# Kernel tuning notes

Hardware: AMD Instinct MI355X
Metric: run time of the kernel (lower is better)

The kernel has to match this reference:

```python
import jax, jax.numpy as jnp
import numpy as np

B, T, N, E = 4, 16, 1024, 16384
F_IN, H, FF, NH, L, C = 128, 256, 1024, 8, 2, 10
HD = H // NH
EPS = 1e-5


def setup_inputs() -> dict:
    key = jax.random.key(0)
    ks = jax.random.split(key, 12)
    g = lambda k, s: jax.random.normal(k, s, dtype=jnp.float32) * 0.02
    return {
        "x": jax.random.normal(ks[0], (B, T, N, F_IN), dtype=jnp.float32),
        "edge_index": jax.random.randint(ks[1], (B, T, 2, E), 0, N, dtype=jnp.int32),
        # GraphSAGE layer 1 (PyG SAGEConv: lin_l on mean-aggregated neighbors, lin_r on self)
        "sage1_Wl": g(ks[2], (F_IN, H)), "sage1_bl": jnp.zeros((H,), jnp.float32),
        "sage1_Wr": g(ks[3], (F_IN, H)),
        # GraphSAGE layer 2
        "sage2_Wl": g(ks[4], (H, H)), "sage2_bl": jnp.zeros((H,), jnp.float32),
        "sage2_Wr": g(ks[5], (H, H)),
        # TransformerEncoder, stacked over L layers
        "Wqkv": g(ks[6], (L, H, 3 * H)), "bqkv": jnp.zeros((L, 3 * H), jnp.float32),
        "Wo": g(ks[7], (L, H, H)), "bo": jnp.zeros((L, H), jnp.float32),
        "ln1_s": jnp.ones((L, H), jnp.float32), "ln1_b": jnp.zeros((L, H), jnp.float32),
        "W1": g(ks[8], (L, H, FF)), "b1": jnp.zeros((L, FF), jnp.float32),
        "W2": g(ks[9], (L, FF, H)), "b2": jnp.zeros((L, H), jnp.float32),
        "ln2_s": jnp.ones((L, H), jnp.float32), "ln2_b": jnp.zeros((L, H), jnp.float32),
        # final classifier
        "fc_W": g(ks[10], (H, C)), "fc_b": jnp.zeros((C,), jnp.float32),
    }


def _sage_conv(x, src, dst, Wl, bl, Wr):
    # mean neighbor aggregation: for each target node, mean of source features
    deg = jax.ops.segment_sum(jnp.ones((E,), x.dtype), dst, num_segments=N)
    agg = jax.ops.segment_sum(x[src], dst, num_segments=N)  # [N, F]
    agg = agg / jnp.clip(deg, 1.0)[:, None]
    return agg @ Wl + bl + x @ Wr


def _layernorm(x, s, b):
    m = jnp.mean(x, axis=-1, keepdims=True)
    v = jnp.var(x, axis=-1, keepdims=True)
    return (x - m) * jax.lax.rsqrt(v + EPS) * s + b


def _encoder_layer(h, Wqkv, bqkv, Wo, bo, ln1_s, ln1_b, W1, b1, W2, b2, ln2_s, ln2_b):
    # h: [B, T, H] -- post-norm (PyTorch default norm_first=False), relu FFN
    qkv = h @ Wqkv + bqkv  # [B, T, 3H]
    q, k, v = jnp.split(qkv, 3, axis=-1)
    sp = lambda t: t.reshape(B, T, NH, HD).transpose(0, 2, 1, 3)  # [B, NH, T, HD]
    q, k, v = sp(q), sp(k), sp(v)
    scores = jnp.einsum("bhqd,bhkd->bhqk", q, k) / np.sqrt(HD).astype(np.float32)
    attn = jax.nn.softmax(scores, axis=-1)
    ctx = jnp.einsum("bhqk,bhkd->bhqd", attn, v)
    ctx = ctx.transpose(0, 2, 1, 3).reshape(B, T, H)
    h = _layernorm(h + ctx @ Wo + bo, ln1_s, ln1_b)
    ffn = jax.nn.relu(h @ W1 + b1) @ W2 + b2
    return _layernorm(h + ffn, ln2_s, ln2_b)


def reference(x, edge_index, sage1_Wl, sage1_bl, sage1_Wr, sage2_Wl, sage2_bl,
              sage2_Wr, Wqkv, bqkv, Wo, bo, ln1_s, ln1_b, W1, b1, W2, b2,
              ln2_s, ln2_b, fc_W, fc_b):
    xf = x.reshape(B * T, N, F_IN)
    ef = edge_index.reshape(B * T, 2, E)

    def per_graph(xg, eg):
        src, dst = eg[0], eg[1]
        h = jax.nn.relu(_sage_conv(xg, src, dst, sage1_Wl, sage1_bl, sage1_Wr))
        h = _sage_conv(h, src, dst, sage2_Wl, sage2_bl, sage2_Wr)
        return jnp.mean(h, axis=0)  # mean-pool over nodes -> [H]

    emb = jax.vmap(per_graph)(xf, ef).reshape(B, T, H)

    h = emb
    for l in range(L):
        h = _encoder_layer(h, Wqkv[l], bqkv[l], Wo[l], bo[l], ln1_s[l], ln1_b[l],
                           W1[l], b1[l], W2[l], b2[l], ln2_s[l], ln2_b[l])
    return h[:, -1, :] @ fc_W + fc_b  # [B, C]
```

## Files before the change

### kernel.cpp

```cpp
#include <hip/hip_runtime.h>
#include <hip/hip_bf16.h>

#define Bc 4
#define Tc 16
#define Nc 1024
#define Ec 16384
#define FIN 128
#define Hc 256
#define FFc 1024
#define NHc 8
#define Lc 2
#define HDc 32
#define Gc 64
#define EPSc 1e-5f

typedef __bf16 v8bf __attribute__((ext_vector_type(8)));
typedef float v4f __attribute__((ext_vector_type(4)));

__global__ void pack_w_kernel(const float* __restrict__ Wl, const float* __restrict__ Wr,
                              __bf16* __restrict__ pH, __bf16* __restrict__ pL) {
    int bid = blockIdx.x;
    int t = threadIdx.x;
    int lane = t >> 3, j = t & 7;
    int kc = bid >> 4, nt = bid & 15;
    int k = kc * 32 + ((lane >> 4) << 3) + j;
    int n = nt * 16 + (lane & 15);
    float w = (k < 128) ? Wl[(size_t)k * Hc + n] : Wr[(size_t)(k - 128) * Hc + n];
    __bf16 hi = (__bf16)w;
    __bf16 lo = (__bf16)(w - (float)hi);
    pH[bid * 512 + t] = hi;
    pL[bid * 512 + t] = lo;
}

__global__ __launch_bounds__(1024) void csr_kernel(
        const int* __restrict__ ei, float* __restrict__ invdeg, float* __restrict__ cw,
        int* __restrict__ off, unsigned short* __restrict__ elist, float* __restrict__ uv) {
    __shared__ int degs[Nc];
    __shared__ float inv[Nc];
    __shared__ float cl[Nc];
    __shared__ int wsum[16];
    int g = blockIdx.x, t = threadIdx.x;
    const int* src = ei + (size_t)g * 2 * Ec;
    const int* dst = src + Ec;
    if (t < 512) uv[g * 512 + t] = 0.f;
    degs[t] = 0; cl[t] = 0.f;
    __syncthreads();
    for (int e = t; e < Ec; e += 1024) atomicAdd(&degs[dst[e] & (Nc - 1)], 1);
    __syncthreads();
    float iv = 1.0f / fmaxf((float)degs[t], 1.0f);
    inv[t] = iv;
    invdeg[g * Nc + t] = iv;
    __syncthreads();
    for (int e = t; e < Ec; e += 1024) atomicAdd(&cl[src[e] & (Nc - 1)], inv[dst[e] & (Nc - 1)]);
    __syncthreads();
    cw[g * Nc + t] = cl[t];
    int own = degs[t];
    int lane = t & 63, wv = t >> 6;
    int val = own;
#pragma unroll
    for (int ofs = 1; ofs < 64; ofs <<= 1) {
        int v = __shfl_up(val, ofs, 64);
        if (lane >= ofs) val += v;
    }
    if (lane == 63) wsum[wv] = val;
    __syncthreads();
    if (wv == 0 && lane < 16) {
        int wval = wsum[lane];
#pragma unroll
        for (int ofs = 1; ofs < 16; ofs <<= 1) {
            int v = __shfl_up(wval, ofs, 64);
            if (lane >= ofs) wval += v;
        }
        wsum[lane] = wval;
    }
    __syncthreads();
    int incl = val + ((wv > 0) ? wsum[wv - 1] : 0);
    int excl = incl - own;
    off[g * 1032 + t] = excl;
    if (t == 1023) off[g * 1032 + Nc] = incl;
    degs[t] = excl;
    __syncthreads();
    for (int e = t; e < Ec; e += 1024) {
        int d = dst[e] & (Nc - 1);
        int slot = atomicAdd(&degs[d], 1);
        elist[(size_t)g * Ec + slot] = (unsigned short)(src[e] & (Nc - 1));
    }
}

__global__ __launch_bounds__(512) void sage_kernel(
        const float* __restrict__ x, const unsigned short* __restrict__ elist,
        const int* __restrict__ off, const float* __restrict__ invdeg,
        const float* __restrict__ cw, const __bf16* __restrict__ pH,
        const __bf16* __restrict__ pL, const float* __restrict__ bias,
        float* __restrict__ uv) {
    __shared__ float aggL[32 * 132];
    __shared__ float xL[32 * 132];
    __shared__ float lu[256], lv[256];
    int tid = threadIdx.x;
    int bid = blockIdx.x;
    int g = bid & 63, cc = bid >> 6, r0 = cc * 32;
    const unsigned short* el = elist + (size_t)g * Ec;
    const float* xg = x + (size_t)g * Nc * FIN;
    if (tid < 256) { lu[tid] = 0.f; lv[tid] = 0.f; }

    {
        int lr = tid >> 4, ch = tid & 15;
        int n = r0 + lr;
        int o0 = off[g * 1032 + n], o1 = off[g * 1032 + n + 1];
        float4 a0 = make_float4(0.f, 0.f, 0.f, 0.f);
        float4 a1 = make_float4(0.f, 0.f, 0.f, 0.f);
        const float* xc = xg + ch * 8;
        int e = o0;
        for (; e + 8 <= o1; e += 8) {
            int s[8];
#pragma unroll
            for (int j = 0; j < 8; ++j) s[j] = el[e + j];
            float4 v0[8], v1[8];
#pragma unroll
            for (int j = 0; j < 8; ++j) {
                const float4* xp = (const float4*)(xc + (size_t)s[j] * FIN);
                v0[j] = xp[0]; v1[j] = xp[1];
            }
#pragma unroll
            for (int j = 0; j < 8; ++j) {
                a0.x += v0[j].x; a0.y += v0[j].y; a0.z += v0[j].z; a0.w += v0[j].w;
                a1.x += v1[j].x; a1.y += v1[j].y; a1.z += v1[j].z; a1.w += v1[j].w;
            }
        }
        for (; e < o1; ++e) {
            const float4* xp = (const float4*)(xc + (size_t)el[e] * FIN);
            float4 v0 = xp[0], v1 = xp[1];
            a0.x += v0.x; a0.y += v0.y; a0.z += v0.z; a0.w += v0.w;
            a1.x += v1.x; a1.y += v1.y; a1.z += v1.z; a1.w += v1.w;
        }
        float iv = invdeg[g * Nc + n];
        float* dp = &aggL[lr * 132 + ch * 8];
        dp[0] = a0.x * iv; dp[1] = a0.y * iv; dp[2] = a0.z * iv; dp[3] = a0.w * iv;
        dp[4] = a1.x * iv; dp[5] = a1.y * iv; dp[6] = a1.z * iv; dp[7] = a1.w * iv;
    }
    for (int i = tid; i < 1024; i += 512) {
        int lr = i >> 5, kq = i & 31;
        *(float4*)&xL[lr * 132 + kq * 4] = *(const float4*)&xg[(size_t)(r0 + lr) * FIN + kq * 4];
    }
    __syncthreads();

    int w = tid >> 6, lane = tid & 63, quad = lane >> 4;
    int mt = w & 1, nh = w >> 1;
    int lrow = mt * 16 + (lane & 15);
    v4f acc[4];
#pragma unroll
    for (int i = 0; i < 4; ++i) acc[i] = (v4f)0.f;
    for (int kc = 0; kc < 8; ++kc) {
        const float* ap = (kc < 4) ? &aggL[lrow * 132 + kc * 32 + quad * 8]
                                   : &xL[lrow * 132 + (kc - 4) * 32 + quad * 8];
        float4 f0 = *(const float4*)ap;
        float4 f1 = *(const float4*)(ap + 4);
        float av[8] = {f0.x, f0.y, f0.z, f0.w, f1.x, f1.y, f1.z, f1.w};
        v8bf aH, aL;
#pragma unroll
        for (int j = 0; j < 8; ++j) {
            __bf16 hb = (__bf16)av[j];
            aH[j] = hb;
            aL[j] = (__bf16)(av[j] - (float)hb);
        }
#pragma unroll
        for (int i = 0; i < 4; ++i) {
            int nt = nh * 4 + i;
            v8bf bH = *(const v8bf*)(pH + ((size_t)(kc * 16 + nt) * 64 + lane) * 8);
            v8bf bL = *(const v8bf*)(pL + ((size_t)(kc * 16 + nt) * 64 + lane) * 8);
            acc[i] = __builtin_amdgcn_mfma_f32_16x16x32_bf16(aH, bH, acc[i], 0, 0, 0);
            acc[i] = __builtin_amdgcn_mfma_f32_16x16x32_bf16(aL, bH, acc[i], 0, 0, 0);
            acc[i] = __builtin_amdgcn_mfma_f32_16x16x32_bf16(aH, bL, acc[i], 0, 0, 0);
        }
    }

    float c4[4];
    int nb = g * Nc + r0 + mt * 16 + quad * 4;
#pragma unroll
    for (int r = 0; r < 4; ++r) c4[r] = cw[nb + r];
#pragma unroll
    for (int i = 0; i < 4; ++i) {
        int col = (nh * 4 + i) * 16 + (lane & 15);
        float bcol = bias[col];
        float su = 0.f, sv = 0.f;
#pragma unroll
        for (int r = 0; r < 4; ++r) {
            float val = fmaxf(acc[i][r] + bcol, 0.f);
            sv += val;
            su += c4[r] * val;
        }
        su += __shfl_xor(su, 16); sv += __shfl_xor(sv, 16);
        su += __shfl_xor(su, 32); sv += __shfl_xor(sv, 32);
        if (quad == 0) { atomicAdd(&lu[col], su); atomicAdd(&lv[col], sv); }
    }
    __syncthreads();
    if (tid < 256) {
        atomicAdd(&uv[g * 512 + tid], lu[tid]);
        atomicAdd(&uv[g * 512 + 256 + tid], lv[tid]);
    }
}

__global__ __launch_bounds__(512) void emb_kernel(
        const float* __restrict__ uv, const float* __restrict__ Wl2,
        const float* __restrict__ bl2, const float* __restrict__ Wr2,
        float* __restrict__ h) {
    __shared__ float s[512];
    __shared__ float r2[512];
    int g = blockIdx.x, tid = threadIdx.x;
    s[tid] = uv[g * 512 + tid] * (1.0f / Nc);
    __syncthreads();
    int col = tid & 255, p = tid >> 8;
    float val = 0.f;
    if (p == 0) { for (int k = 0; k < 256; ++k) val += s[k] * Wl2[(size_t)k * Hc + col]; }
    else        { for (int k = 0; k < 256; ++k) val += s[256 + k] * Wr2[(size_t)k * Hc + col]; }
    r2[tid] = val;
    __syncthreads();
    if (tid < 256) h[g * Hc + tid] = bl2[tid] + r2[tid] + r2[tid + 256];
}

__global__ __launch_bounds__(512) void qkv_kernel(
        const float* __restrict__ h, const float* __restrict__ Wqkv,
        const float* __restrict__ bqkv, float* __restrict__ qkv, int l) {
    __shared__ float hr[256];
    __shared__ float r2[512];
    int bid = blockIdx.x;
    int gi = bid / 3, seg = bid % 3;
    int tid = threadIdx.x;
    if (tid < 256) hr[tid] = h[gi * Hc + tid];
    __syncthreads();
    int col = seg * 256 + (tid & 255);
    int half = tid >> 8;
    const float* W = Wqkv + (size_t)l * Hc * 768;
    float val = 0.f;
    int k0 = half * 128;
    for (int k = 0; k < 128; ++k) val += hr[k0 + k] * W[(size_t)(k0 + k) * 768 + col];
    r2[tid] = val;
    __syncthreads();
    if (tid < 256) qkv[gi * 768 + col] = bqkv[(size_t)l * 768 + col] + r2[tid] + r2[tid + 256];
}

#define KVS 516
__global__ __launch_bounds__(512) void apl_kernel(
        const float* __restrict__ h, const float* __restrict__ qkvg,
        const float* __restrict__ Wo, const float* __restrict__ bo,
        const float* __restrict__ s1, const float* __restrict__ b1ln,
        float* __restrict__ h1buf, int l) {
    __shared__ float kv[16 * KVS];
    __shared__ float q[256];
    __shared__ float sc[8][17];
    __shared__ float ctx[256];
    __shared__ float r2[512];
    __shared__ float red[256];
    int t = blockIdx.x, tid = threadIdx.x;
    int b = t >> 4;
    const float* qb = qkvg + (size_t)(b * 16) * 768;
    for (int i = tid; i < 8192; i += 512) {
        int j = i >> 9, d = i & 511;
        kv[j * KVS + d] = qb[(size_t)j * 768 + 256 + d];
    }
    if (tid < 256) q[tid] = qkvg[(size_t)t * 768 + tid];
    __syncthreads();
    if (tid < 128) {
        int hd = tid >> 4, j = tid & 15;
        float s = 0.f;
#pragma unroll
        for (int d = 0; d < 32; ++d) s += q[hd * 32 + d] * kv[j * KVS + hd * 32 + d];
        sc[hd][j] = s * 0.17677669529663687f;
    }
    __syncthreads();
    if (tid < 8) {
        float m = sc[tid][0];
        for (int j = 1; j < 16; ++j) m = fmaxf(m, sc[tid][j]);
        float e[16], sum = 0.f;
        for (int j = 0; j < 16; ++j) { e[j] = expf(sc[tid][j] - m); sum += e[j]; }
        float inv = 1.0f / sum;
        for (int j = 0; j < 16; ++j) sc[tid][j] = e[j] * inv;
    }
    __syncthreads();
    if (tid < 256) {
        int hd = tid >> 5, d = tid & 31;
        float o = 0.f;
#pragma unroll
        for (int j = 0; j < 16; ++j) o += sc[hd][j] * kv[j * KVS + 256 + hd * 32 + d];
        ctx[tid] = o;
    }
    __syncthreads();
    int col = tid & 255, half = tid >> 8;
    const float* W = Wo + (size_t)l * 65536;
    float pv = 0.f;
    int k0 = half * 128;
    for (int k = 0; k < 128; ++k) pv += ctx[k0 + k] * W[(size_t)(k0 + k) * 256 + col];
    r2[tid] = pv;
    __syncthreads();
    float val = 0.f;
    if (tid < 256) {
        val = h[(size_t)t * 256 + tid] + bo[(size_t)l * 256 + tid] + r2[tid] + r2[tid + 256];
        red[tid] = val;
    }
    __syncthreads();
    for (int s = 128; s > 0; s >>= 1) { if (tid < s) red[tid] += red[tid + s]; __syncthreads(); }
    float m1 = red[0] * (1.0f / 256.0f);
    __syncthreads();
    float d1 = val - m1;
    if (tid < 256) red[tid] = d1 * d1;
    __syncthreads();
    for (int s = 128; s > 0; s >>= 1) { if (tid < s) red[tid] += red[tid + s]; __syncthreads(); }
    float v1 = red[0] * (1.0f / 256.0f);
    if (tid < 256)
        h1buf[(size_t)t * 256 + tid] =
            d1 * rsqrtf(v1 + EPSc) * s1[(size_t)l * 256 + tid] + b1ln[(size_t)l * 256 + tid];
}

__global__ __launch_bounds__(512) void ffn1_kernel(
        const float* __restrict__ h1buf, const float* __restrict__ W1,
        const float* __restrict__ bf1, float* __restrict__ fL, int l) {
    __shared__ float hr[256];
    __shared__ float r2[512];
    int bid = blockIdx.x;
    int t = bid >> 2, cg = bid & 3;
    int tid = threadIdx.x;
    if (tid < 256) hr[tid] = h1buf[(size_t)t * 256 + tid];
    __syncthreads();
    int col = cg * 256 + (tid & 255);
    int half = tid >> 8;
    const float* W = W1 + (size_t)l * 262144;
    float val = 0.f;
    int k0 = half * 128;
    for (int k = 0; k < 128; ++k) val += hr[k0 + k] * W[(size_t)(k0 + k) * 1024 + col];
    r2[tid] = val;
    __syncthreads();
    if (tid < 256)
        fL[(size_t)t * 1024 + col] = fmaxf(bf1[(size_t)l * 1024 + col] + r2[tid] + r2[tid + 256], 0.f);
}

__global__ __launch_bounds__(1024) void ffn2_ln_kernel(
        float* __restrict__ h, const float* __restrict__ h1buf, const float* __restrict__ fL,
        const float* __restrict__ W2, const float* __restrict__ bf2,
        const float* __restrict__ s2, const float* __restrict__ b2ln,
        const float* __restrict__ fcW, const float* __restrict__ fcb,
        float* __restrict__ out, int l, int last) {
    __shared__ float fs[1024];
    __shared__ float r4[1024];
    __shared__ float red[256];
    int t = blockIdx.x, tid = threadIdx.x;
    fs[tid] = fL[(size_t)t * 1024 + tid];
    __syncthreads();
    int col = tid & 255, kq = tid >> 8;
    const float* W = W2 + (size_t)l * 262144;
    float p = 0.f;
    int k0 = kq * 256;
    for (int k = 0; k < 256; ++k) p += fs[k0 + k] * W[(size_t)(k0 + k) * 256 + col];
    r4[tid] = p;
    __syncthreads();
    float val = 0.f;
    if (tid < 256) {
        val = h1buf[(size_t)t * 256 + tid] + bf2[(size_t)l * 256 + tid]
            + r4[tid] + r4[tid + 256] + r4[tid + 512] + r4[tid + 768];
        red[tid] = val;
    }
    __syncthreads();
    for (int s = 128; s > 0; s >>= 1) { if (tid < s) red[tid] += red[tid + s]; __syncthreads(); }
    float m2 = red[0] * (1.0f / 256.0f);
    __syncthreads();
    float d2 = (tid < 256) ? (val - m2) : 0.f;
    if (tid < 256) red[tid] = d2 * d2;
    __syncthreads();
    for (int s = 128; s > 0; s >>= 1) { if (tid < s) red[tid] += red[tid + s]; __syncthreads(); }
    float var2 = red[0] * (1.0f / 256.0f);
    float hn = 0.f;
    if (tid < 256) {
        hn = d2 * rsqrtf(var2 + EPSc) * s2[(size_t)l * 256 + tid] + b2ln[(size_t)l * 256 + tid];
        h[(size_t)t * 256 + tid] = hn;
    }
    if (last && (t & 15) == 15) {
        __syncthreads();
        if (tid < 256) red[tid] = hn;
        __syncthreads();
        if (tid < 10) {
            int b = t >> 4;
            float fv = fcb[tid];
            for (int k = 0; k < 256; ++k) fv += red[k] * fcW[(size_t)k * 10 + tid];
            out[b * 10 + tid] = fv;
        }
    }
}

extern "C" void kernel_launch(void* const* d_in, const int* in_sizes, int n_in,
                              void* d_out, int out_size, void* d_ws, size_t ws_size,
                              hipStream_t stream) {
    (void)in_sizes; (void)n_in; (void)out_size; (void)ws_size;
    const float* x    = (const float*)d_in[0];
    const int*   ei   = (const int*)d_in[1];
    const float* s1Wl = (const float*)d_in[2];
    const float* s1bl = (const float*)d_in[3];
    const float* s1Wr = (const float*)d_in[4];
    const float* s2Wl = (const float*)d_in[5];
    const float* s2bl = (const float*)d_in[6];
    const float* s2Wr = (const float*)d_in[7];
    const float* Wqkv = (const float*)d_in[8];
    const float* bqkv = (const float*)d_in[9];
    const float* Wo   = (const float*)d_in[10];
    const float* bo   = (const float*)d_in[11];
    const float* ln1s = (const float*)d_in[12];
    const float* ln1b = (const float*)d_in[13];
    const float* W1   = (const float*)d_in[14];
    const float* b1   = (const float*)d_in[15];
    const float* W2   = (const float*)d_in[16];
    const float* b2   = (const float*)d_in[17];
    const float* ln2s = (const float*)d_in[18];
    const float* ln2b = (const float*)d_in[19];
    const float* fcW  = (const float*)d_in[20];
    const float* fcb  = (const float*)d_in[21];

    char* ws = (char*)d_ws;
    __bf16*         packWH = (__bf16*)(ws + 0);
    __bf16*         packWL = (__bf16*)(ws + 131072);
    float*          invdeg = (float*)(ws + 262144);
    float*          cw     = (float*)(ws + 524288);
    int*            off    = (int*)(ws + 786432);
    unsigned short* elist  = (unsigned short*)(ws + 1050624);
    float*          uv     = (float*)(ws + 3147776);
    float*          h      = (float*)(ws + 3278848);
    float*          qkvg   = (float*)(ws + 3344384);
    float*          h1buf  = (float*)(ws + 3540992);
    float*          fLbuf  = (float*)(ws + 3606528);

    pack_w_kernel<<<128, 512, 0, stream>>>(s1Wl, s1Wr, packWH, packWL);
    csr_kernel<<<Gc, 1024, 0, stream>>>(ei, invdeg, cw, off, elist, uv);
    sage_kernel<<<Gc * 32, 512, 0, stream>>>(x, elist, off, invdeg, cw, packWH, packWL, s1bl, uv);
    emb_kernel<<<Gc, 512, 0, stream>>>(uv, s2Wl, s2bl, s2Wr, h);
    for (int l = 0; l < Lc; ++l) {
        qkv_kernel<<<Gc * 3, 512, 0, stream>>>(h, Wqkv, bqkv, qkvg, l);
        apl_kernel<<<Gc, 512, 0, stream>>>(h, qkvg, Wo, bo, ln1s, ln1b, h1buf, l);
        ffn1_kernel<<<Gc * 4, 512, 0, stream>>>(h1buf, W1, b1, fLbuf, l);
        ffn2_ln_kernel<<<Gc, 1024, 0, stream>>>(h, h1buf, fLbuf, W2, b2, ln2s, ln2b,
                                                fcW, fcb, (float*)d_out, l, l == Lc - 1);
    }
}
```

Baseline: 321.1 us.

## Pipeline SAGE neighbor gather through LDS with async global_load_lds

Reworks the neighbor aggregation in sage_kernel. Each wave now owns 4 rows and streams the source-node feature rows into a 4-slot LDS ring using global_load_lds, with manual vmcnt waits keeping several loads in flight. The edge list for the block is first staged into shared memory, and the self-feature tile is also loaded asynchronously with global_load_lds; an old per-thread gather remains as a fallback when a block has more than 1024 edges. The aim is to hide gather latency and issue wider coalesced loads, at the cost of more shared memory (about 70KB, which lowers occupancy) and hand-written waitcnt logic.

```diff
diff --git a/kernel.cpp b/kernel.cpp
--- a/kernel.cpp
+++ b/kernel.cpp
@@ -16,6 +16,10 @@
 
 typedef __bf16 v8bf __attribute__((ext_vector_type(8)));
 typedef float v4f __attribute__((ext_vector_type(4)));
+
+#define GLOAD_LDS16(gp, lp) \
+    __builtin_amdgcn_global_load_lds((const __attribute__((address_space(1))) void*)(gp), \
+                                     (__attribute__((address_space(3))) void*)(lp), 16, 0, 0)
 
 __global__ void pack_w_kernel(const float* __restrict__ Wl, const float* __restrict__ Wr,
                               __bf16* __restrict__ pH, __bf16* __restrict__ pL) {
@@ -93,42 +97,103 @@
         const float* __restrict__ cw, const __bf16* __restrict__ pH,
         const __bf16* __restrict__ pL, const float* __restrict__ bias,
         float* __restrict__ uv) {
-    __shared__ float aggL[32 * 132];
-    __shared__ float xL[32 * 132];
-    __shared__ float lu[256], lv[256];
+    __shared__ __align__(16) float smem[17570];
+    float* aggL = smem;
+    float* xL = smem + 4224;
+    float* stage = smem + 8320;
+    float* lu = smem + 16512;
+    float* lv = smem + 16768;
+    float* invS = smem + 17024;
+    unsigned short* elS = (unsigned short*)(smem + 17056);
+
     int tid = threadIdx.x;
     int bid = blockIdx.x;
     int g = bid & 63, cc = bid >> 6, r0 = cc * 32;
     const unsigned short* el = elist + (size_t)g * Ec;
     const float* xg = x + (size_t)g * Nc * FIN;
+    int wv = tid >> 6, lane = tid & 63;
+
+#pragma unroll
+    for (int k = 0; k < 2; ++k) {
+        int rr = 4 * wv + 2 * k;
+        const float* gp = xg + (size_t)(r0 + rr) * FIN + lane * 4;
+        GLOAD_LDS16(gp, &xL[rr * FIN]);
+    }
+
+    int ob = g * 1032 + r0;
+    int eb0 = off[ob];
+    int eend = off[ob + 32];
+    int cnt = eend - eb0;
+    bool fb = (cnt > 1024);
+
     if (tid < 256) { lu[tid] = 0.f; lv[tid] = 0.f; }
-
-    {
+    if (tid < 32) invS[tid] = invdeg[g * Nc + r0 + tid];
+    if (!fb) {
+        for (int i = tid; i < cnt + 2; i += 512) elS[i] = el[eb0 + i];
+    }
+    int rw0 = r0 + 4 * wv;
+    int oA  = off[g * 1032 + rw0];
+    int oE1 = off[g * 1032 + rw0 + 1];
+    int oE2 = off[g * 1032 + rw0 + 2];
+    int oE3 = off[g * 1032 + rw0 + 3];
+    int oE4 = off[g * 1032 + rw0 + 4];
+    __syncthreads();
+
+    if (!fb) {
+        float* myst = &stage[wv * 1024];
+        int ebase = oA;
+        int nE = oE4 - oA;
+        int np = (nE + 1) >> 1;
+        float ax = 0.f, ay = 0.f;
+        int r = 0;
+        int bnd = oE1;
+
+        auto ISSUE = [&](int p) {
+            int e0 = ebase + 2 * p;
+            int s = elS[e0 - eb0 + (lane >> 5)] & (Nc - 1);
+            const float* gp = xg + (size_t)s * FIN + (lane & 31) * 4;
+            GLOAD_LDS16(gp, myst + (p & 3) * 256);
+        };
+        auto WOUT = [&]() {
+            float iv = invS[4 * wv + r];
+            int arow = 4 * wv + r;
+            *(float2*)&aggL[arow * 132 + 2 * lane] = make_float2(ax * iv, ay * iv);
+            ax = 0.f; ay = 0.f;
+            ++r;
+            bnd = (r == 1) ? oE2 : (r == 2) ? oE3 : oE4;
+        };
+
+        if (np > 0) ISSUE(0);
+        if (np > 1) ISSUE(1);
+        if (np > 2) ISSUE(2);
+        int e = ebase;
+        for (int p = 0; p < np; ++p) {
+            int rem = np - 1 - p;
+            if (rem >= 2)      asm volatile("s_waitcnt vmcnt(2)" ::: "memory");
+            else if (rem == 1) asm volatile("s_waitcnt vmcnt(1)" ::: "memory");
+            else               asm volatile("s_waitcnt vmcnt(0)" ::: "memory");
+            const float* sp = myst + (p & 3) * 256;
+#pragma unroll
+            for (int j = 0; j < 2; ++j) {
+                while (r < 4 && e >= bnd) WOUT();
+                if (e < oE4) {
+                    float2 v = *(const float2*)&sp[j * 128 + 2 * lane];
+                    ax += v.x; ay += v.y;
+                }
+                ++e;
+            }
+            if (p + 3 < np) ISSUE(p + 3);
+        }
+        while (r < 4) WOUT();
+    } else {
         int lr = tid >> 4, ch = tid & 15;
         int n = r0 + lr;
         int o0 = off[g * 1032 + n], o1 = off[g * 1032 + n + 1];
         float4 a0 = make_float4(0.f, 0.f, 0.f, 0.f);
         float4 a1 = make_float4(0.f, 0.f, 0.f, 0.f);
         const float* xc = xg + ch * 8;
-        int e = o0;
-        for (; e + 8 <= o1; e += 8) {
-            int s[8];
-#pragma unroll
-            for (int j = 0; j < 8; ++j) s[j] = el[e + j];
-            float4 v0[8], v1[8];
-#pragma unroll
-            for (int j = 0; j < 8; ++j) {
-                const float4* xp = (const float4*)(xc + (size_t)s[j] * FIN);
-                v0[j] = xp[0]; v1[j] = xp[1];
-            }
-#pragma unroll
-            for (int j = 0; j < 8; ++j) {
-                a0.x += v0[j].x; a0.y += v0[j].y; a0.z += v0[j].z; a0.w += v0[j].w;
-                a1.x += v1[j].x; a1.y += v1[j].y; a1.z += v1[j].z; a1.w += v1[j].w;
-            }
-        }
-        for (; e < o1; ++e) {
-            const float4* xp = (const float4*)(xc + (size_t)el[e] * FIN);
+        for (int e2 = o0; e2 < o1; ++e2) {
+            const float4* xp = (const float4*)(xc + (size_t)el[e2] * FIN);
             float4 v0 = xp[0], v1 = xp[1];
             a0.x += v0.x; a0.y += v0.y; a0.z += v0.z; a0.w += v0.w;
             a1.x += v1.x; a1.y += v1.y; a1.z += v1.z; a1.w += v1.w;
@@ -138,13 +203,9 @@
         dp[0] = a0.x * iv; dp[1] = a0.y * iv; dp[2] = a0.z * iv; dp[3] = a0.w * iv;
         dp[4] = a1.x * iv; dp[5] = a1.y * iv; dp[6] = a1.z * iv; dp[7] = a1.w * iv;
     }
-    for (int i = tid; i < 1024; i += 512) {
-        int lr = i >> 5, kq = i & 31;
-        *(float4*)&xL[lr * 132 + kq * 4] = *(const float4*)&xg[(size_t)(r0 + lr) * FIN + kq * 4];
-    }
-    __syncthreads();
-
-    int w = tid >> 6, lane = tid & 63, quad = lane >> 4;
+    __syncthreads();
+
+    int w = wv, quad = lane >> 4;
     int mt = w & 1, nh = w >> 1;
     int lrow = mt * 16 + (lane & 15);
     v4f acc[4];
@@ -152,7 +213,7 @@
     for (int i = 0; i < 4; ++i) acc[i] = (v4f)0.f;
     for (int kc = 0; kc < 8; ++kc) {
         const float* ap = (kc < 4) ? &aggL[lrow * 132 + kc * 32 + quad * 8]
-                                   : &xL[lrow * 132 + (kc - 4) * 32 + quad * 8];
+                                   : &xL[lrow * 128 + (kc - 4) * 32 + quad * 8];
         float4 f0 = *(const float4*)ap;
         float4 f1 = *(const float4*)(ap + 4);
         float av[8] = {f0.x, f0.y, f0.z, f0.w, f1.x, f1.y, f1.z, f1.w};
@@ -177,17 +238,17 @@
     float c4[4];
     int nb = g * Nc + r0 + mt * 16 + quad * 4;
 #pragma unroll
-    for (int r = 0; r < 4; ++r) c4[r] = cw[nb + r];
+    for (int rr = 0; rr < 4; ++rr) c4[rr] = cw[nb + rr];
 #pragma unroll
     for (int i = 0; i < 4; ++i) {
         int col = (nh * 4 + i) * 16 + (lane & 15);
         float bcol = bias[col];
         float su = 0.f, sv = 0.f;
 #pragma unroll
-        for (int r = 0; r < 4; ++r) {
-            float val = fmaxf(acc[i][r] + bcol, 0.f);
+        for (int rr = 0; rr < 4; ++rr) {
+            float val = fmaxf(acc[i][rr] + bcol, 0.f);
             sv += val;
-            su += c4[r] * val;
+            su += c4[rr] * val;
         }
         su += __shfl_xor(su, 16); sv += __shfl_xor(sv, 16);
         su += __shfl_xor(su, 32); sv += __shfl_xor(sv, 32);
```

Result: slower. 573.5 us (+78.6%).

## Pipeline SAGE neighbor gather per wave with LDS-staged edge list

Applied to the files above, without the earlier changes.

The neighbor aggregation in the SAGE kernel now stages the block's edge indices into shared memory, then has each wave walk the edges of 4 consecutive nodes. Each lane loads a float2 covering the full 128-wide feature row, with a 16-deep software pipeline of in-flight loads and index prefetch, flushing accumulators at node boundaries. The self-feature tile load is moved ahead of the gather so it overlaps with it. The aim is more memory-level parallelism and coalesced row reads, replacing the old 16-thread-per-row scheme. This costs more registers and branchy boundary handling, and keeps a fallback path for blocks with more than 1024 edges.

```diff
diff --git a/kernel.cpp b/kernel.cpp
--- a/kernel.cpp
+++ b/kernel.cpp
@@ -96,39 +96,121 @@
     __shared__ float aggL[32 * 132];
     __shared__ float xL[32 * 132];
     __shared__ float lu[256], lv[256];
+    __shared__ float invS[32];
+    __shared__ unsigned short elS[1024];
     int tid = threadIdx.x;
     int bid = blockIdx.x;
     int g = bid & 63, cc = bid >> 6, r0 = cc * 32;
     const unsigned short* el = elist + (size_t)g * Ec;
     const float* xg = x + (size_t)g * Nc * FIN;
+    int wv = tid >> 6, lane = tid & 63;
     if (tid < 256) { lu[tid] = 0.f; lv[tid] = 0.f; }
-
-    {
+    if (tid < 32) invS[tid] = invdeg[g * Nc + r0 + tid];
+
+    int ob = g * 1032 + r0;
+    int eb0 = off[ob];
+    int cnt = off[ob + 32] - eb0;
+    bool fb = (cnt > 1024);
+    if (!fb) {
+        for (int i = tid; i < cnt; i += 512) elS[i] = el[eb0 + i];
+    }
+    for (int i = tid; i < 1024; i += 512) {
+        int lr = i >> 5, kq = i & 31;
+        *(float4*)&xL[lr * 132 + kq * 4] = *(const float4*)&xg[(size_t)(r0 + lr) * FIN + kq * 4];
+    }
+    int rw0 = r0 + 4 * wv;
+    int oA  = off[g * 1032 + rw0];
+    int oE1 = off[g * 1032 + rw0 + 1];
+    int oE2 = off[g * 1032 + rw0 + 2];
+    int oE3 = off[g * 1032 + rw0 + 3];
+    int oE4 = off[g * 1032 + rw0 + 4];
+    __syncthreads();
+
+    if (!fb) {
+        int qA = oA - eb0;
+        int m  = oE4 - oA;
+        float ax = 0.f, ay = 0.f;
+        int r = 0, bnd = oE1;
+        const float* xl2 = xg + (lane << 1);
+        float2 s0, s1, s2, s3, s4, s5, s6, s7;
+        float2 u0, u1, u2, u3, u4, u5, u6, u7;
+        int iA0, iA1, iA2, iA3, iA4, iA5, iA6, iA7;
+        int iB0, iB1, iB2, iB3, iB4, iB5, iB6, iB7;
+
+#define FLUSHW() { float iv_ = invS[(wv << 2) + r]; \
+        *(float2*)&aggL[((wv << 2) + r) * 132 + (lane << 1)] = \
+            make_float2(ax * iv_, ay * iv_); \
+        ax = 0.f; ay = 0.f; ++r; \
+        bnd = (r == 1) ? oE2 : (r == 2) ? oE3 : (r == 3) ? oE4 : 0x7fffffff; }
+#define RD(NK, J) NK = ((J) < m) ? (int)elS[qA + (J)] : 0;
+#define ISS(SK, NK, J) if ((J) < m) SK = *(const float2*)(xl2 + ((NK) << 7));
+#define CONSUME(SK, J) { int eg_ = oA + (J); \
+        while (r < 4 && eg_ >= bnd) FLUSHW(); \
+        ax += SK.x; ay += SK.y; }
+
+        {
+            int t0, t1, t2, t3, t4, t5, t6, t7;
+            RD(t0, 0) RD(t1, 1) RD(t2, 2) RD(t3, 3) RD(t4, 4) RD(t5, 5) RD(t6, 6) RD(t7, 7)
+            ISS(s0, t0, 0) ISS(s1, t1, 1) ISS(s2, t2, 2) ISS(s3, t3, 3)
+            ISS(s4, t4, 4) ISS(s5, t5, 5) ISS(s6, t6, 6) ISS(s7, t7, 7)
+            RD(t0, 8) RD(t1, 9) RD(t2, 10) RD(t3, 11) RD(t4, 12) RD(t5, 13) RD(t6, 14) RD(t7, 15)
+            ISS(u0, t0, 8) ISS(u1, t1, 9) ISS(u2, t2, 10) ISS(u3, t3, 11)
+            ISS(u4, t4, 12) ISS(u5, t5, 13) ISS(u6, t6, 14) ISS(u7, t7, 15)
+        }
+        RD(iA0, 16) RD(iA1, 17) RD(iA2, 18) RD(iA3, 19)
+        RD(iA4, 20) RD(iA5, 21) RD(iA6, 22) RD(iA7, 23)
+        RD(iB0, 24) RD(iB1, 25) RD(iB2, 26) RD(iB3, 27)
+        RD(iB4, 28) RD(iB5, 29) RD(iB6, 30) RD(iB7, 31)
+
+        int jb = 0;
+        for (; jb + 16 <= m; jb += 16) {
+            CONSUME(s0, jb + 0)  ISS(s0, iA0, jb + 16) RD(iA0, jb + 32)
+            CONSUME(s1, jb + 1)  ISS(s1, iA1, jb + 17) RD(iA1, jb + 33)
+            CONSUME(s2, jb + 2)  ISS(s2, iA2, jb + 18) RD(iA2, jb + 34)
+            CONSUME(s3, jb + 3)  ISS(s3, iA3, jb + 19) RD(iA3, jb + 35)
+            CONSUME(s4, jb + 4)  ISS(s4, iA4, jb + 20) RD(iA4, jb + 36)
+            CONSUME(s5, jb + 5)  ISS(s5, iA5, jb + 21) RD(iA5, jb + 37)
+            CONSUME(s6, jb + 6)  ISS(s6, iA6, jb + 22) RD(iA6, jb + 38)
+            CONSUME(s7, jb + 7)  ISS(s7, iA7, jb + 23) RD(iA7, jb + 39)
+            CONSUME(u0, jb + 8)  ISS(u0, iB0, jb + 24) RD(iB0, jb + 40)
+            CONSUME(u1, jb + 9)  ISS(u1, iB1, jb + 25) RD(iB1, jb + 41)
+            CONSUME(u2, jb + 10) ISS(u2, iB2, jb + 26) RD(iB2, jb + 42)
+            CONSUME(u3, jb + 11) ISS(u3, iB3, jb + 27) RD(iB3, jb + 43)
+            CONSUME(u4, jb + 12) ISS(u4, iB4, jb + 28) RD(iB4, jb + 44)
+            CONSUME(u5, jb + 13) ISS(u5, iB5, jb + 29) RD(iB5, jb + 45)
+            CONSUME(u6, jb + 14) ISS(u6, iB6, jb + 30) RD(iB6, jb + 46)
+            CONSUME(u7, jb + 15) ISS(u7, iB7, jb + 31) RD(iB7, jb + 47)
+        }
+        if (jb + 0 < m)  CONSUME(s0, jb + 0)
+        if (jb + 1 < m)  CONSUME(s1, jb + 1)
+        if (jb + 2 < m)  CONSUME(s2, jb + 2)
+        if (jb + 3 < m)  CONSUME(s3, jb + 3)
+        if (jb + 4 < m)  CONSUME(s4, jb + 4)
+        if (jb + 5 < m)  CONSUME(s5, jb + 5)
+        if (jb + 6 < m)  CONSUME(s6, jb + 6)
+        if (jb + 7 < m)  CONSUME(s7, jb + 7)
+        if (jb + 8 < m)  CONSUME(u0, jb + 8)
+        if (jb + 9 < m)  CONSUME(u1, jb + 9)
+        if (jb + 10 < m) CONSUME(u2, jb + 10)
+        if (jb + 11 < m) CONSUME(u3, jb + 11)
+        if (jb + 12 < m) CONSUME(u4, jb + 12)
+        if (jb + 13 < m) CONSUME(u5, jb + 13)
+        if (jb + 14 < m) CONSUME(u6, jb + 14)
+        if (jb + 15 < m) CONSUME(u7, jb + 15)
+        while (r < 4) FLUSHW();
+#undef FLUSHW
+#undef RD
+#undef ISS
+#undef CONSUME
+    } else {
         int lr = tid >> 4, ch = tid & 15;
         int n = r0 + lr;
         int o0 = off[g * 1032 + n], o1 = off[g * 1032 + n + 1];
         float4 a0 = make_float4(0.f, 0.f, 0.f, 0.f);
         float4 a1 = make_float4(0.f, 0.f, 0.f, 0.f);
         const float* xc = xg + ch * 8;
-        int e = o0;
-        for (; e + 8 <= o1; e += 8) {
-            int s[8];
-#pragma unroll
-            for (int j = 0; j < 8; ++j) s[j] = el[e + j];
-            float4 v0[8], v1[8];
-#pragma unroll
-            for (int j = 0; j < 8; ++j) {
-                const float4* xp = (const float4*)(xc + (size_t)s[j] * FIN);
-                v0[j] = xp[0]; v1[j] = xp[1];
-            }
-#pragma unroll
-            for (int j = 0; j < 8; ++j) {
-                a0.x += v0[j].x; a0.y += v0[j].y; a0.z += v0[j].z; a0.w += v0[j].w;
-                a1.x += v1[j].x; a1.y += v1[j].y; a1.z += v1[j].z; a1.w += v1[j].w;
-            }
-        }
-        for (; e < o1; ++e) {
-            const float4* xp = (const float4*)(xc + (size_t)el[e] * FIN);
+        for (int e2 = o0; e2 < o1; ++e2) {
+            const float4* xp = (const float4*)(xc + (size_t)el[e2] * FIN);
             float4 v0 = xp[0], v1 = xp[1];
             a0.x += v0.x; a0.y += v0.y; a0.z += v0.z; a0.w += v0.w;
             a1.x += v1.x; a1.y += v1.y; a1.z += v1.z; a1.w += v1.w;
@@ -138,13 +220,9 @@
         dp[0] = a0.x * iv; dp[1] = a0.y * iv; dp[2] = a0.z * iv; dp[3] = a0.w * iv;
         dp[4] = a1.x * iv; dp[5] = a1.y * iv; dp[6] = a1.z * iv; dp[7] = a1.w * iv;
     }
-    for (int i = tid; i < 1024; i += 512) {
-        int lr = i >> 5, kq = i & 31;
-        *(float4*)&xL[lr * 132 + kq * 4] = *(const float4*)&xg[(size_t)(r0 + lr) * FIN + kq * 4];
-    }
-    __syncthreads();
-
-    int w = tid >> 6, lane = tid & 63, quad = lane >> 4;
+    __syncthreads();
+
+    int w = wv, quad = lane >> 4;
     int mt = w & 1, nh = w >> 1;
     int lrow = mt * 16 + (lane & 15);
     v4f acc[4];
@@ -177,17 +255,17 @@
     float c4[4];
     int nb = g * Nc + r0 + mt * 16 + quad * 4;
 #pragma unroll
-    for (int r = 0; r < 4; ++r) c4[r] = cw[nb + r];
+    for (int rr = 0; rr < 4; ++rr) c4[rr] = cw[nb + rr];
 #pragma unroll
     for (int i = 0; i < 4; ++i) {
         int col = (nh * 4 + i) * 16 + (lane & 15);
         float bcol = bias[col];
         float su = 0.f, sv = 0.f;
 #pragma unroll
-        for (int r = 0; r < 4; ++r) {
-            float val = fmaxf(acc[i][r] + bcol, 0.f);
+        for (int rr = 0; rr < 4; ++rr) {
+            float val = fmaxf(acc[i][rr] + bcol, 0.f);
             sv += val;
-            su += c4[r] * val;
+            su += c4[rr] * val;
         }
         su += __shfl_xor(su, 16); sv += __shfl_xor(sv, 16);
         su += __shfl_xor(su, 32); sv += __shfl_xor(sv, 32);
```

New measurement: 339.4 us. 5.7% more time.

## Fuse each transformer encoder layer into a single kernel launch

Applied to the files above, without the earlier changes.

Replaces the four per-layer kernels (qkv, attention+proj+LN, FFN1, FFN2+LN) with one 1024-thread kernel per layer. Each block recomputes the K/V projections for all 16 timesteps of its batch from a transposed copy of h held in shared memory, so the qkv, h1 and FFN intermediates no longer round-trip through global memory. This cuts six launches and their global-memory handoffs. The cost is redundant K/V computation, 16x per batch, and only 64 blocks doing the FFN matmuls instead of up to 256.

```diff
diff --git a/kernel.cpp b/kernel.cpp
--- a/kernel.cpp
+++ b/kernel.cpp
@@ -218,54 +218,73 @@
     if (tid < 256) h[g * Hc + tid] = bl2[tid] + r2[tid] + r2[tid + 256];
 }
 
-__global__ __launch_bounds__(512) void qkv_kernel(
-        const float* __restrict__ h, const float* __restrict__ Wqkv,
-        const float* __restrict__ bqkv, float* __restrict__ qkv, int l) {
-    __shared__ float hr[256];
-    __shared__ float r2[512];
-    int bid = blockIdx.x;
-    int gi = bid / 3, seg = bid % 3;
-    int tid = threadIdx.x;
-    if (tid < 256) hr[tid] = h[gi * Hc + tid];
-    __syncthreads();
-    int col = seg * 256 + (tid & 255);
-    int half = tid >> 8;
-    const float* W = Wqkv + (size_t)l * Hc * 768;
-    float val = 0.f;
-    int k0 = half * 128;
-    for (int k = 0; k < 128; ++k) val += hr[k0 + k] * W[(size_t)(k0 + k) * 768 + col];
-    r2[tid] = val;
-    __syncthreads();
-    if (tid < 256) qkv[gi * 768 + col] = bqkv[(size_t)l * 768 + col] + r2[tid] + r2[tid + 256];
-}
-
-#define KVS 516
-__global__ __launch_bounds__(512) void apl_kernel(
-        const float* __restrict__ h, const float* __restrict__ qkvg,
+__global__ __launch_bounds__(1024) void layer_kernel(
+        const float* __restrict__ hin, float* __restrict__ hout,
+        const float* __restrict__ Wqkv, const float* __restrict__ bqkv,
         const float* __restrict__ Wo, const float* __restrict__ bo,
         const float* __restrict__ s1, const float* __restrict__ b1ln,
-        float* __restrict__ h1buf, int l) {
-    __shared__ float kv[16 * KVS];
+        const float* __restrict__ W1, const float* __restrict__ bf1,
+        const float* __restrict__ W2, const float* __restrict__ bf2,
+        const float* __restrict__ s2, const float* __restrict__ b2ln,
+        const float* __restrict__ fcW, const float* __restrict__ fcb,
+        float* __restrict__ out, int l, int last) {
+    __shared__ float hT[256 * 16];
+    __shared__ float kvL[16 * 512];
     __shared__ float q[256];
     __shared__ float sc[8][17];
     __shared__ float ctx[256];
     __shared__ float r2[512];
     __shared__ float red[256];
+    __shared__ float rF[2048];
+    __shared__ float fLs[1024];
+    __shared__ float h1L[256];
     int t = blockIdx.x, tid = threadIdx.x;
-    int b = t >> 4;
-    const float* qb = qkvg + (size_t)(b * 16) * 768;
-    for (int i = tid; i < 8192; i += 512) {
-        int j = i >> 9, d = i & 511;
-        kv[j * KVS + d] = qb[(size_t)j * 768 + 256 + d];
-    }
-    if (tid < 256) q[tid] = qkvg[(size_t)t * 768 + tid];
+    int b = t >> 4, own = t & 15;
+    for (int i = tid; i < 4096; i += 1024) {
+        int j = i >> 8, k = i & 255;
+        hT[k * 16 + j] = hin[(size_t)(b * 16 + j) * 256 + k];
+    }
+    __syncthreads();
+    {
+        int col = tid & 511, jh = tid >> 9;
+        const float* W = Wqkv + (size_t)l * Hc * 768 + 256 + col;
+        float acc[8], s0[8];
+#pragma unroll
+        for (int j = 0; j < 8; ++j) acc[j] = 0.f;
+        for (int k = 0; k < 128; ++k) {
+            float w = W[(size_t)k * 768];
+            const float4* hk = (const float4*)&hT[k * 16 + jh * 8];
+            float4 h0 = hk[0], h1 = hk[1];
+            acc[0] += h0.x * w; acc[1] += h0.y * w; acc[2] += h0.z * w; acc[3] += h0.w * w;
+            acc[4] += h1.x * w; acc[5] += h1.y * w; acc[6] += h1.z * w; acc[7] += h1.w * w;
+        }
+#pragma unroll
+        for (int j = 0; j < 8; ++j) { s0[j] = acc[j]; acc[j] = 0.f; }
+        for (int k = 128; k < 256; ++k) {
+            float w = W[(size_t)k * 768];
+            const float4* hk = (const float4*)&hT[k * 16 + jh * 8];
+            float4 h0 = hk[0], h1 = hk[1];
+            acc[0] += h0.x * w; acc[1] += h0.y * w; acc[2] += h0.z * w; acc[3] += h0.w * w;
+            acc[4] += h1.x * w; acc[5] += h1.y * w; acc[6] += h1.z * w; acc[7] += h1.w * w;
+        }
+        float bq = bqkv[(size_t)l * 768 + 256 + col];
+#pragma unroll
+        for (int j = 0; j < 8; ++j) kvL[(size_t)(jh * 8 + j) * 512 + col] = bq + s0[j] + acc[j];
+    }
+    if (tid < 256) {
+        const float* W = Wqkv + (size_t)l * Hc * 768 + tid;
+        float p0 = 0.f, p1 = 0.f;
+        for (int k = 0; k < 128; ++k) p0 += hT[k * 16 + own] * W[(size_t)k * 768];
+        for (int k = 128; k < 256; ++k) p1 += hT[k * 16 + own] * W[(size_t)k * 768];
+        q[tid] = bqkv[(size_t)l * 768 + tid] + p0 + p1;
+    }
     __syncthreads();
     if (tid < 128) {
-        int hd = tid >> 4, j = tid & 15;
+        int hd = tid >> 4, jj = tid & 15;
         float s = 0.f;
 #pragma unroll
-        for (int d = 0; d < 32; ++d) s += q[hd * 32 + d] * kv[j * KVS + hd * 32 + d];
-        sc[hd][j] = s * 0.17677669529663687f;
+        for (int d = 0; d < 32; ++d) s += q[hd * 32 + d] * kvL[jj * 512 + hd * 32 + d];
+        sc[hd][jj] = s * 0.17677669529663687f;
     }
     __syncthreads();
     if (tid < 8) {
@@ -281,20 +300,22 @@
         int hd = tid >> 5, d = tid & 31;
         float o = 0.f;
 #pragma unroll
-        for (int j = 0; j < 16; ++j) o += sc[hd][j] * kv[j * KVS + 256 + hd * 32 + d];
+        for (int j = 0; j < 16; ++j) o += sc[hd][j] * kvL[j * 512 + 256 + hd * 32 + d];
         ctx[tid] = o;
     }
     __syncthreads();
-    int col = tid & 255, half = tid >> 8;
-    const float* W = Wo + (size_t)l * 65536;
-    float pv = 0.f;
-    int k0 = half * 128;
-    for (int k = 0; k < 128; ++k) pv += ctx[k0 + k] * W[(size_t)(k0 + k) * 256 + col];
-    r2[tid] = pv;
+    if (tid < 512) {
+        int col = tid & 255, half = tid >> 8;
+        const float* W = Wo + (size_t)l * 65536;
+        float pv = 0.f;
+        int k0 = half * 128;
+        for (int k = 0; k < 128; ++k) pv += ctx[k0 + k] * W[(size_t)(k0 + k) * 256 + col];
+        r2[tid] = pv;
+    }
     __syncthreads();
     float val = 0.f;
     if (tid < 256) {
-        val = h[(size_t)t * 256 + tid] + bo[(size_t)l * 256 + tid] + r2[tid] + r2[tid + 256];
+        val = hT[tid * 16 + own] + bo[(size_t)l * 256 + tid] + r2[tid] + r2[tid + 256];
         red[tid] = val;
     }
     __syncthreads();
@@ -307,62 +328,45 @@
     for (int s = 128; s > 0; s >>= 1) { if (tid < s) red[tid] += red[tid + s]; __syncthreads(); }
     float v1 = red[0] * (1.0f / 256.0f);
     if (tid < 256)
-        h1buf[(size_t)t * 256 + tid] =
-            d1 * rsqrtf(v1 + EPSc) * s1[(size_t)l * 256 + tid] + b1ln[(size_t)l * 256 + tid];
-}
-
-__global__ __launch_bounds__(512) void ffn1_kernel(
-        const float* __restrict__ h1buf, const float* __restrict__ W1,
-        const float* __restrict__ bf1, float* __restrict__ fL, int l) {
-    __shared__ float hr[256];
-    __shared__ float r2[512];
-    int bid = blockIdx.x;
-    int t = bid >> 2, cg = bid & 3;
-    int tid = threadIdx.x;
-    if (tid < 256) hr[tid] = h1buf[(size_t)t * 256 + tid];
-    __syncthreads();
-    int col = cg * 256 + (tid & 255);
-    int half = tid >> 8;
-    const float* W = W1 + (size_t)l * 262144;
-    float val = 0.f;
-    int k0 = half * 128;
-    for (int k = 0; k < 128; ++k) val += hr[k0 + k] * W[(size_t)(k0 + k) * 1024 + col];
-    r2[tid] = val;
-    __syncthreads();
-    if (tid < 256)
-        fL[(size_t)t * 1024 + col] = fmaxf(bf1[(size_t)l * 1024 + col] + r2[tid] + r2[tid + 256], 0.f);
-}
-
-__global__ __launch_bounds__(1024) void ffn2_ln_kernel(
-        float* __restrict__ h, const float* __restrict__ h1buf, const float* __restrict__ fL,
-        const float* __restrict__ W2, const float* __restrict__ bf2,
-        const float* __restrict__ s2, const float* __restrict__ b2ln,
-        const float* __restrict__ fcW, const float* __restrict__ fcb,
-        float* __restrict__ out, int l, int last) {
-    __shared__ float fs[1024];
-    __shared__ float r4[1024];
-    __shared__ float red[256];
-    int t = blockIdx.x, tid = threadIdx.x;
-    fs[tid] = fL[(size_t)t * 1024 + tid];
-    __syncthreads();
-    int col = tid & 255, kq = tid >> 8;
-    const float* W = W2 + (size_t)l * 262144;
-    float p = 0.f;
-    int k0 = kq * 256;
-    for (int k = 0; k < 256; ++k) p += fs[k0 + k] * W[(size_t)(k0 + k) * 256 + col];
-    r4[tid] = p;
-    __syncthreads();
-    float val = 0.f;
-    if (tid < 256) {
-        val = h1buf[(size_t)t * 256 + tid] + bf2[(size_t)l * 256 + tid]
-            + r4[tid] + r4[tid + 256] + r4[tid + 512] + r4[tid + 768];
-        red[tid] = val;
+        h1L[tid] = d1 * rsqrtf(v1 + EPSc) * s1[(size_t)l * 256 + tid] + b1ln[(size_t)l * 256 + tid];
+    __syncthreads();
+#pragma unroll
+    for (int pass = 0; pass < 2; ++pass) {
+        int pid = pass * 1024 + tid;
+        int cg = pid >> 9, ch = pid & 511;
+        int col = cg * 256 + (ch & 255), half = ch >> 8;
+        const float* W = W1 + (size_t)l * 262144;
+        float v = 0.f;
+        int k0 = half * 128;
+        for (int k = 0; k < 128; ++k) v += h1L[k0 + k] * W[(size_t)(k0 + k) * 1024 + col];
+        rF[pid] = v;
+    }
+    __syncthreads();
+    {
+        int cg = tid >> 8, c8 = tid & 255;
+        fLs[tid] = fmaxf(bf1[(size_t)l * 1024 + tid] + rF[cg * 512 + c8] + rF[cg * 512 + 256 + c8], 0.f);
+    }
+    __syncthreads();
+    {
+        int col = tid & 255, kq = tid >> 8;
+        const float* W = W2 + (size_t)l * 262144;
+        float p = 0.f;
+        int k0 = kq * 256;
+        for (int k = 0; k < 256; ++k) p += fLs[k0 + k] * W[(size_t)(k0 + k) * 256 + col];
+        rF[tid] = p;
+    }
+    __syncthreads();
+    float val2 = 0.f;
+    if (tid < 256) {
+        val2 = h1L[tid] + bf2[(size_t)l * 256 + tid]
+             + rF[tid] + rF[tid + 256] + rF[tid + 512] + rF[tid + 768];
+        red[tid] = val2;
     }
     __syncthreads();
     for (int s = 128; s > 0; s >>= 1) { if (tid < s) red[tid] += red[tid + s]; __syncthreads(); }
     float m2 = red[0] * (1.0f / 256.0f);
     __syncthreads();
-    float d2 = (tid < 256) ? (val - m2) : 0.f;
+    float d2 = (tid < 256) ? (val2 - m2) : 0.f;
     if (tid < 256) red[tid] = d2 * d2;
     __syncthreads();
     for (int s = 128; s > 0; s >>= 1) { if (tid < s) red[tid] += red[tid + s]; __syncthreads(); }
@@ -370,14 +374,13 @@
     float hn = 0.f;
     if (tid < 256) {
         hn = d2 * rsqrtf(var2 + EPSc) * s2[(size_t)l * 256 + tid] + b2ln[(size_t)l * 256 + tid];
-        h[(size_t)t * 256 + tid] = hn;
-    }
-    if (last && (t & 15) == 15) {
+        hout[(size_t)t * 256 + tid] = hn;
+    }
+    if (last && own == 15) {
         __syncthreads();
         if (tid < 256) red[tid] = hn;
         __syncthreads();
         if (tid < 10) {
-            int b = t >> 4;
             float fv = fcb[tid];
             for (int k = 0; k < 256; ++k) fv += red[k] * fcW[(size_t)k * 10 + tid];
             out[b * 10 + tid] = fv;
@@ -421,19 +424,16 @@
     unsigned short* elist  = (unsigned short*)(ws + 1050624);
     float*          uv     = (float*)(ws + 3147776);
     float*          h      = (float*)(ws + 3278848);
-    float*          qkvg   = (float*)(ws + 3344384);
-    float*          h1buf  = (float*)(ws + 3540992);
-    float*          fLbuf  = (float*)(ws + 3606528);
+    float*          h2     = (float*)(ws + 3344384);
 
     pack_w_kernel<<<128, 512, 0, stream>>>(s1Wl, s1Wr, packWH, packWL);
     csr_kernel<<<Gc, 1024, 0, stream>>>(ei, invdeg, cw, off, elist, uv);
     sage_kernel<<<Gc * 32, 512, 0, stream>>>(x, elist, off, invdeg, cw, packWH, packWL, s1bl, uv);
     emb_kernel<<<Gc, 512, 0, stream>>>(uv, s2Wl, s2bl, s2Wr, h);
-    for (int l = 0; l < Lc; ++l) {
-        qkv_kernel<<<Gc * 3, 512, 0, stream>>>(h, Wqkv, bqkv, qkvg, l);
-        apl_kernel<<<Gc, 512, 0, stream>>>(h, qkvg, Wo, bo, ln1s, ln1b, h1buf, l);
-        ffn1_kernel<<<Gc * 4, 512, 0, stream>>>(h1buf, W1, b1, fLbuf, l);
-        ffn2_ln_kernel<<<Gc, 1024, 0, stream>>>(h, h1buf, fLbuf, W2, b2, ln2s, ln2b,
-                                                fcW, fcb, (float*)d_out, l, l == Lc - 1);
-    }
-}
+    layer_kernel<<<Gc, 1024, 0, stream>>>(h, h2, Wqkv, bqkv, Wo, bo, ln1s, ln1b,
+                                          W1, b1, W2, b2, ln2s, ln2b, fcW, fcb,
+                                          (float*)d_out, 0, 0);
+    layer_kernel<<<Gc, 1024, 0, stream>>>(h2, h, Wqkv, bqkv, Wo, bo, ln1s, ln1b,
+                                          W1, b1, W2, b2, ln2s, ln2b, fcW, fcb,
+                                          (float*)d_out, 1, 1);
+}
```

Result: slower. 346.0 us (+7.7%).
